# Kernel optimization log

Hardware: AMD Instinct MI355X
Metric: run time of the kernel (lower is better)

The kernel has to match this reference:

```python
import jax, jax.numpy as jnp
import numpy as np

N = 50000      # nodes
E = 800000     # edges
DIN = 128
DH = 128
DE = 128
DOUT = 2
EPS = 1e-5     # GraphNorm eps


def _xavier(key, fan_in, fan_out):
    lim = float(np.sqrt(6.0 / (fan_in + fan_out)))
    return jax.random.uniform(key, (fan_in, fan_out), jnp.float32, -lim, lim)


def setup_inputs() -> dict:
    key = jax.random.key(0)
    ks = jax.random.split(key, 8)
    x = jax.random.normal(ks[0], (N, DIN), jnp.float32)
    edge_index = jax.random.randint(ks[1], (2, E), 0, N, dtype=jnp.int32)
    W1 = _xavier(ks[2], DIN, DH); b1 = jnp.zeros((DH,), jnp.float32)
    W2 = _xavier(ks[3], DH, DH);  b2 = jnp.zeros((DH,), jnp.float32)
    W3 = _xavier(ks[4], DH, DE);  b3 = jnp.zeros((DE,), jnp.float32)
    gn1_w = jnp.ones((DH,), jnp.float32); gn1_b = jnp.zeros((DH,), jnp.float32); gn1_a = jnp.ones((DH,), jnp.float32)
    gn2_w = jnp.ones((DH,), jnp.float32); gn2_b = jnp.zeros((DH,), jnp.float32); gn2_a = jnp.ones((DH,), jnp.float32)
    Wout = _xavier(ks[5], DE, DOUT); bout = jnp.zeros((DOUT,), jnp.float32)
    return {
        "x": x, "edge_index": edge_index,
        "W1": W1, "b1": b1, "W2": W2, "b2": b2, "W3": W3, "b3": b3,
        "gn1_w": gn1_w, "gn1_b": gn1_b, "gn1_a": gn1_a,
        "gn2_w": gn2_w, "gn2_b": gn2_b, "gn2_a": gn2_a,
        "Wout": Wout, "bout": bout,
    }


def gcn_conv(x, src, dst, W, b):
    # PyG GCNConv: add self-loops, symmetric normalization, linear, scatter-add at dst.
    n = x.shape[0]
    h = x @ W                                   # [N, C]
    loop = jnp.arange(n, dtype=src.dtype)
    s = jnp.concatenate([src, loop])            # [E+N]
    d = jnp.concatenate([dst, loop])
    deg = jnp.zeros((n,), h.dtype).at[d].add(1.0)
    dinv = jnp.where(deg > 0, jax.lax.rsqrt(deg), 0.0)
    norm = dinv[s] * dinv[d]                    # [E+N]
    out = jnp.zeros_like(h).at[d].add(h[s] * norm[:, None])
    return out + b


def graph_norm(h, w, b, alpha):
    # Single-graph GraphNorm: shift by alpha*mean, normalize by variance of shifted values.
    mean = h.mean(axis=0)
    c = h - alpha * mean
    var = (c * c).mean(axis=0)
    return c * jax.lax.rsqrt(var + EPS) * w + b


def reference(x, edge_index, W1, b1, W2, b2, W3, b3,
              gn1_w, gn1_b, gn1_a, gn2_w, gn2_b, gn2_a, Wout, bout):
    src, dst = edge_index[0], edge_index[1]
    h = gcn_conv(x, src, dst, W1, b1)
    h = jax.nn.relu(graph_norm(h, gn1_w, gn1_b, gn1_a))   # dropout identity (eval)
    h = gcn_conv(h, src, dst, W2, b2)
    h = jax.nn.relu(graph_norm(h, gn2_w, gn2_b, gn2_a))
    h = gcn_conv(h, src, dst, W3, b3)
    return h @ Wout + bout
```

## Files before the change

kernel.cpp:

```cpp
#include <hip/hip_runtime.h>

#define GN_EPS 1e-5f


typedef __attribute__((ext_vector_type(8))) short short8;
typedef __attribute__((ext_vector_type(4))) float f32x4;

__device__ __forceinline__ unsigned short f2bf(float f) {
    unsigned u = __float_as_uint(f);
    u += 0x7fffu + ((u >> 16) & 1u);
    return (unsigned short)(u >> 16);
}
__device__ __forceinline__ float bflo(unsigned u) { return __uint_as_float(u << 16); }
__device__ __forceinline__ float bfhi(unsigned u) { return __uint_as_float(u & 0xffff0000u); }

__global__ void k_degi(const int* __restrict__ dst, int* __restrict__ degi,
                       unsigned short* __restrict__ slot, int e) {
    int i = blockIdx.x * blockDim.x + threadIdx.x;
    if (i < e) slot[i] = (unsigned short)atomicAdd(&degi[dst[i]], 1);
}

#define SCAN_CHUNK 4096
__global__ __launch_bounds__(256) void k_blocksum(const int* __restrict__ degi,
                                                  int* __restrict__ partial, int n) {
    int base = blockIdx.x * SCAN_CHUNK + threadIdx.x * 16;
    int s = 0;
    #pragma unroll
    for (int q = 0; q < 16; ++q) {
        int i = base + q;
        if (i < n) s += (degi[i] + 15) & ~15;
    }
    #pragma unroll
    for (int off = 32; off; off >>= 1) s += __shfl_down(s, off);
    __shared__ int ws[4];
    if ((threadIdx.x & 63) == 0) ws[threadIdx.x >> 6] = s;
    __syncthreads();
    if (threadIdx.x == 0) partial[blockIdx.x] = ws[0] + ws[1] + ws[2] + ws[3];
}

__global__ __launch_bounds__(256) void k_scanfinal(const int* __restrict__ degi,
                                                   const int* __restrict__ partial,
                                                   int* __restrict__ rowptr,
                                                   float* __restrict__ dinv, int n, int nb) {
    int blockbase = 0;
    for (int i = 0; i < (int)blockIdx.x; ++i) blockbase += partial[i];

    int base = blockIdx.x * SCAN_CHUNK + threadIdx.x * 16;
    int v[16], pv[16];
    int s = 0;
    #pragma unroll
    for (int q = 0; q < 16; ++q) {
        int i = base + q;
        v[q] = (i < n) ? degi[i] : 0;
        pv[q] = (v[q] + 15) & ~15;
        s += pv[q];
    }
    const int lane = threadIdx.x & 63;
    const int wid = threadIdx.x >> 6;
    int x = s;
    #pragma unroll
    for (int off = 1; off < 64; off <<= 1) {
        int t = __shfl_up(x, off);
        if (lane >= off) x += t;
    }
    __shared__ int ws[4];
    if (lane == 63) ws[wid] = x;
    __syncthreads();
    int waveoff = 0;
    if (wid > 0) waveoff += ws[0];
    if (wid > 1) waveoff += ws[1];
    if (wid > 2) waveoff += ws[2];
    int excl = x - s + waveoff + blockbase;
    #pragma unroll
    for (int q = 0; q < 16; ++q) {
        int i = base + q;
        if (i < n) {
            rowptr[i] = excl;
            dinv[i] = rsqrtf((float)(v[q] + 1));
        }
        excl += pv[q];
    }
    if ((int)blockIdx.x == nb - 1 && threadIdx.x == 255) {
        rowptr[n] = excl;
    }
}

__global__ void k_fill(const int* __restrict__ src, const int* __restrict__ dst,
                       const unsigned short* __restrict__ slot, const int* __restrict__ rowptr,
                       const float* __restrict__ dinv,
                       unsigned* __restrict__ csr_ew, int e) {
    int i = blockIdx.x * blockDim.x + threadIdx.x;
    if (i < e) {
        int s = src[i], d = dst[i];
        float w = dinv[s] * dinv[d];
        csr_ew[rowptr[d] + (int)slot[i]] = ((unsigned)s << 16) | (unsigned)f2bf(w);
    }
}

__global__ __launch_bounds__(256) void k_prep(const float* __restrict__ W1,
                                              const float* __restrict__ W2,
                                              const float* __restrict__ W3,
                                              const float* __restrict__ Wo,
                                              const float* __restrict__ b3,
                                              const float* __restrict__ bo,
                                              unsigned short* __restrict__ Wt,
                                              float* __restrict__ M,
                                              float* __restrict__ mb) {
    __shared__ unsigned short sT[128 * 130];
    if (blockIdx.x < 2) {
        const float* W = blockIdx.x == 0 ? W1 : W2;
        unsigned short* o = Wt + blockIdx.x * 16384;
        const float4* W4 = (const float4*)W;
        for (int idx = threadIdx.x; idx < 128 * 32; idx += 256) {
            int k = idx >> 5, c4 = idx & 31;
            float4 v = W4[k * 32 + c4];
            sT[(c4 * 4 + 0) * 130 + k] = f2bf(v.x);
            sT[(c4 * 4 + 1) * 130 + k] = f2bf(v.y);
            sT[(c4 * 4 + 2) * 130 + k] = f2bf(v.z);
            sT[(c4 * 4 + 3) * 130 + k] = f2bf(v.w);
        }
        __syncthreads();
        for (int idx = threadIdx.x; idx < 128 * 128; idx += 256) {
            int c = idx >> 7, k = idx & 127;
            o[idx] = sT[c * 130 + k];
        }
    } else {
        int k = threadIdx.x;
        if (k < 128) {
            float m0 = 0.f, m1 = 0.f;
            for (int c = 0; c < 128; ++c) {
                float w = W3[k * 128 + c];
                m0 += w * Wo[c * 2];
                m1 += w * Wo[c * 2 + 1];
            }
            M[k * 2] = m0;
            M[k * 2 + 1] = m1;
            if (k < 2) {
                float s = 0.f;
                for (int c = 0; c < 128; ++c) s += b3[c] * Wo[c * 2 + k];
                mb[k] = s + bo[k];
            }
        }
    }
}

#define LDK 136
__global__ __launch_bounds__(256) void k_gemm_f32(const float* __restrict__ X,
                                                  const unsigned short* __restrict__ Wt,
                                                  unsigned short* __restrict__ Y,
                                                  int nrows) {
    __shared__ __align__(16) unsigned short sX[64 * LDK];
    __shared__ __align__(16) unsigned short sB[128 * LDK];
    const int t = threadIdx.x;
    const int row0 = blockIdx.x * 64;

    for (int idx = t; idx < 128 * 16; idx += 256) {
        int c = idx >> 4, ch = idx & 15;
        uint4 v = ((const uint4*)(Wt + c * 128))[ch];
        *(uint4*)(&sB[c * LDK + ch * 8]) = v;
    }
    for (int idx = t; idx < 64 * 32; idx += 256) {
        int r = idx >> 5, c4 = idx & 31;
        int grow = row0 + r;
        float4 v = make_float4(0.f, 0.f, 0.f, 0.f);
        if (grow < nrows) v = ((const float4*)(X + (size_t)grow * 128))[c4];
        ushort4 o;
        o.x = f2bf(v.x); o.y = f2bf(v.y); o.z = f2bf(v.z); o.w = f2bf(v.w);
        *(ushort4*)(&sX[r * LDK + c4 * 4]) = o;
    }
    __syncthreads();

    const int w = t >> 6;
    const int lane = t & 63;
    const int m = lane & 15;
    const int quad = lane >> 4;

    f32x4 acc[8] = {};
    #pragma unroll
    for (int ks = 0; ks < 4; ++ks) {
        int ko = ks * 32 + quad * 8;
        short8 a = *(const short8*)(&sX[(w * 16 + m) * LDK + ko]);
        #pragma unroll
        for (int ct = 0; ct < 8; ++ct) {
            short8 b = *(const short8*)(&sB[(ct * 16 + m) * LDK + ko]);
            acc[ct] = __builtin_amdgcn_mfma_f32_16x16x32_bf16(a, b, acc[ct], 0, 0, 0);
        }
    }
    #pragma unroll
    for (int r = 0; r < 4; ++r) {
        int grow = row0 + w * 16 + quad * 4 + r;
        if (grow >= nrows) continue;
        unsigned short* yr = Y + (size_t)grow * 128 + m;
        #pragma unroll
        for (int ct = 0; ct < 8; ++ct) yr[ct * 16] = f2bf(acc[ct][r]);
    }
}

__global__ __launch_bounds__(256) void k_gemm_bf(const unsigned short* __restrict__ Xb,
                                                 const unsigned short* __restrict__ Wt,
                                                 unsigned short* __restrict__ Y,
                                                 const float* __restrict__ cs,
                                                 const float* __restrict__ cb,
                                                 int nrows) {
    __shared__ __align__(16) unsigned short sX[64 * LDK];
    __shared__ __align__(16) unsigned short sB[128 * LDK];
    const int t = threadIdx.x;
    const int row0 = blockIdx.x * 64;
// ... 26 lines not shown

    f32x4 acc[8] = {};
    #pragma unroll
    for (int ks = 0; ks < 4; ++ks) {
        int ko = ks * 32 + quad * 8;
        short8 a = *(const short8*)(&sX[(w * 16 + m) * LDK + ko]);
        #pragma unroll
        for (int ct = 0; ct < 8; ++ct) {
            short8 b = *(const short8*)(&sB[(ct * 16 + m) * LDK + ko]);
            acc[ct] = __builtin_amdgcn_mfma_f32_16x16x32_bf16(a, b, acc[ct], 0, 0, 0);
        }
    }
    #pragma unroll
    for (int r = 0; r < 4; ++r) {
        int grow = row0 + w * 16 + quad * 4 + r;
        if (grow >= nrows) continue;
        unsigned short* yr = Y + (size_t)grow * 128 + m;
        #pragma unroll
        for (int ct = 0; ct < 8; ++ct) yr[ct * 16] = f2bf(acc[ct][r]);
    }
}

__global__ __launch_bounds__(256) void k_gather(const unsigned short* __restrict__ H,
                                                unsigned short* __restrict__ O,
                                                const int* __restrict__ rowptr,
                                                const unsigned* __restrict__ csr_ew,
                                                const float* __restrict__ dinv,
                                                const float* __restrict__ bias,
                                                float* __restrict__ pS,
                                                float* __restrict__ pQ, int n) {
    __shared__ float sS[4][128];
    __shared__ float sQ[4][128];
    const int wid = threadIdx.x >> 6;
    const int node = blockIdx.x * 4 + wid;
    const int lane = threadIdx.x & 63;
    const int qw = lane >> 4;
    const int ql = lane & 15;
    const uint4* Hx = (const uint4*)H;
    float acc[8] = {};
    if (node < n) {
        float di = dinv[node];
        if (qw == 0) {
            uint4 u = Hx[(size_t)node * 16 + ql];
            float dd = di * di;
            float4 ba = ((const float4*)bias)[ql * 2];
            float4 bb = ((const float4*)bias)[ql * 2 + 1];
            acc[0] = bflo(u.x) * dd + ba.x; acc[1] = bfhi(u.x) * dd + ba.y;
            acc[2] = bflo(u.y) * dd + ba.z; acc[3] = bfhi(u.y) * dd + ba.w;
            acc[4] = bflo(u.z) * dd + bb.x; acc[5] = bfhi(u.z) * dd + bb.y;
            acc[6] = bflo(u.w) * dd + bb.z; acc[7] = bfhi(u.w) * dd + bb.w;
        }
        int j = rowptr[node];
        const int end = rowptr[node + 1];
        for (; j < end; j += 16) {
            unsigned ew[4];
            #pragma unroll
            for (int q = 0; q < 4; ++q) ew[q] = csr_ew[j + 4 * q + qw];
            uint4 u[4];
            #pragma unroll
            for (int q = 0; q < 4; ++q) {
                unsigned idx = ((ew[q] >> 12) & 0xFFFF0u) + (unsigned)ql;
                u[q] = Hx[idx];
            }
            #pragma unroll
            for (int q = 0; q < 4; ++q) {
                float nr = __uint_as_float(ew[q] << 16);
                acc[0] += bflo(u[q].x) * nr; acc[1] += bfhi(u[q].x) * nr;
                acc[2] += bflo(u[q].y) * nr; acc[3] += bfhi(u[q].y) * nr;
                acc[4] += bflo(u[q].z) * nr; acc[5] += bfhi(u[q].z) * nr;
                acc[6] += bflo(u[q].w) * nr; acc[7] += bfhi(u[q].w) * nr;
            }
        }
        #pragma unroll
        for (int i = 0; i < 8; ++i) {
            acc[i] += __shfl_down(acc[i], 32);
            acc[i] += __shfl_down(acc[i], 16);
        }
    }
    if (qw == 0) {
        if (node < n) {
            unsigned short h[8];
            float v[8];
            #pragma unroll
            for (int i = 0; i < 8; ++i) {
                h[i] = f2bf(acc[i]);
                v[i] = __uint_as_float((unsigned)h[i] << 16);
                sS[wid][ql * 8 + i] = v[i];
                sQ[wid][ql * 8 + i] = v[i] * v[i];
            }
            uint4 o;
            o.x = (unsigned)h[0] | ((unsigned)h[1] << 16);
            o.y = (unsigned)h[2] | ((unsigned)h[3] << 16);
            o.z = (unsigned)h[4] | ((unsigned)h[5] << 16);
            o.w = (unsigned)h[6] | ((unsigned)h[7] << 16);
            *(uint4*)(O + (size_t)node * 128 + ql * 8) = o;
        } else {
            #pragma unroll
            for (int i = 0; i < 8; ++i) {
                sS[wid][ql * 8 + i] = 0.f;
                sQ[wid][ql * 8 + i] = 0.f;
            }
        }
    }
    __syncthreads();
    const int t = threadIdx.x;
    if (t < 128) {
        float s = sS[0][t] + sS[1][t] + sS[2][t] + sS[3][t];
        float q = sQ[0][t] + sQ[1][t] + sQ[2][t] + sQ[3][t];
        const int slotb = (blockIdx.x & 63) << 7;
        atomicAdd(&pS[slotb + t], s);
        atomicAdd(&pQ[slotb + t], q);
    }
}

__global__ __launch_bounds__(256) void k_zproj(const unsigned short* __restrict__ Xb,
                                               const float* __restrict__ M,
                                               const float* __restrict__ cs,
                                               const float* __restrict__ cb,
                                               float2* __restrict__ Z, int n) {
    int node = blockIdx.x * 4 + (threadIdx.x >> 6);
    if (node >= n) return;
    int lane = threadIdx.x & 63;
    unsigned u = ((const unsigned*)Xb)[(size_t)node * 64 + lane];
// ... 48 lines not shown
        out[(size_t)node * 2 + 1] = acc.y;
    }
}

__global__ void k_finstats(const float* __restrict__ pS, const float* __restrict__ pQ,
                           const float* __restrict__ w, const float* __restrict__ b,
                           const float* __restrict__ alpha,
                           float* __restrict__ colscale, float* __restrict__ colshift,
                           int n) {
    int c = threadIdx.x;
    if (c >= 128) return;
    float s = 0.f, q = 0.f;
    #pragma unroll 8
    for (int blk = 0; blk < 64; ++blk) {
        s += pS[blk * 128 + c];
        q += pQ[blk * 128 + c];
    }
    float inv_n = 1.0f / (float)n;
    float m = s * inv_n;
    float eh2 = q * inv_n;
    float a = alpha[c];
    float var = eh2 - (2.0f * a - a * a) * m * m;
    float scale = rsqrtf(var + GN_EPS) * w[c];
    colscale[c] = scale;
    colshift[c] = b[c] - a * m * scale;
}

extern "C" void kernel_launch(void* const* d_in, const int* in_sizes, int n_in,
                              void* d_out, int out_size, void* d_ws, size_t ws_size,
                              hipStream_t stream) {
    const float* x    = (const float*)d_in[0];
    const int*   ei   = (const int*)  d_in[1];
    const float* W1   = (const float*)d_in[2];
    const float* b1   = (const float*)d_in[3];
    const float* W2   = (const float*)d_in[4];
    const float* b2   = (const float*)d_in[5];
    const float* W3   = (const float*)d_in[6];
    const float* b3   = (const float*)d_in[7];
    const float* gn1w = (const float*)d_in[8];
    const float* gn1b = (const float*)d_in[9];
    const float* gn1a = (const float*)d_in[10];
    const float* gn2w = (const float*)d_in[11];
    const float* gn2b = (const float*)d_in[12];
    const float* gn2a = (const float*)d_in[13];
    const float* Wout = (const float*)d_in[14];
    const float* bout = (const float*)d_in[15];
    float* out = (float*)d_out;

    const int n = in_sizes[0] / 128;
    const int e = in_sizes[1] / 2;
    const int* srcI = ei;
    const int* dstI = ei + e;

    char* base = (char*)d_ws;
    size_t off = 0;
    auto take = [&](size_t bytes) -> void* {
        void* r = base + off;
        off += (bytes + 15) & ~(size_t)15;
        return r;
    };
    unsigned short* bufH = (unsigned short*)take((size_t)n * 256);
    unsigned short* bufG = (unsigned short*)take((size_t)n * 256);
    float* dinv     = (float*)take((size_t)n * 4);
    float* colscale = (float*)take(128 * 4);
    float* colshift = (float*)take(128 * 4);
    int*   rowptr   = (int*)take(((size_t)n + 1) * 4);
    int*   partial  = (int*)take(64 * 4);
    unsigned short* Wt = (unsigned short*)take(2 * 16384 * 2);
    float* M        = (float*)take(256 * 4);
    float* mb       = (float*)take(2 * 4);
    float2* Z       = (float2*)take((size_t)n * 8);
    int*   degi     = (int*)take((size_t)n * 4);
    float* pS       = (float*)take(2 * 64 * 128 * 4);
    float* pQ       = (float*)take(2 * 64 * 128 * 4);
    size_t csr_cap  = (size_t)e + 16 * (size_t)n;
    unsigned* csr_ew = (unsigned*)take(csr_cap * 4);
    size_t zbytes   = (size_t)((base + off) - (char*)degi);

    unsigned short* slot = bufH;

    const int nb = (n + SCAN_CHUNK - 1) / SCAN_CHUNK;

    hipMemsetAsync(degi, 0, zbytes, stream);
    k_degi<<<(e + 255) / 256, 256, 0, stream>>>(dstI, degi, slot, e);
    k_blocksum<<<nb, 256, 0, stream>>>(degi, partial, n);
    k_scanfinal<<<nb, 256, 0, stream>>>(degi, partial, rowptr, dinv, n, nb);
    k_fill<<<(e + 255) / 256, 256, 0, stream>>>(srcI, dstI, slot, rowptr, dinv, csr_ew, e);
    k_prep<<<3, 256, 0, stream>>>(W1, W2, W3, Wout, b3, bout, Wt, M, mb);

    const int gemmGrid = (n + 63) / 64;
    const int gathGrid = (n + 3) / 4;

    k_gemm_f32<<<gemmGrid, 256, 0, stream>>>(x, Wt, bufH, n);
    k_gather<<<gathGrid, 256, 0, stream>>>(bufH, bufG, rowptr, csr_ew, dinv, b1, pS, pQ, n);
    k_finstats<<<1, 128, 0, stream>>>(pS, pQ, gn1w, gn1b, gn1a, colscale, colshift, n);

    k_gemm_bf<<<gemmGrid, 256, 0, stream>>>(bufG, Wt + 16384, bufH, colscale, colshift, n);
    k_gather<<<gathGrid, 256, 0, stream>>>(bufH, bufG, rowptr, csr_ew, dinv, b2,
                                           pS + 8192, pQ + 8192, n);
    k_finstats<<<1, 128, 0, stream>>>(pS + 8192, pQ + 8192, gn2w, gn2b, gn2a,
                                      colscale, colshift, n);

    k_zproj<<<gathGrid, 256, 0, stream>>>(bufG, M, colscale, colshift, Z, n);
    k_gatherZ<<<(n + 15) / 16, 256, 0, stream>>>(Z, rowptr, csr_ew, dinv, mb, out, n);
}
```

Measured before the change: 289.8 us.

## Fuse degree count into prep and CSR fill into first GEMM launch

Merges the weight-prep kernel with the degree-counting atomics, and runs the CSR fill and the first feature GEMM as interleaved block roles of a single launch. The fill now takes slot positions from a per-row atomic cursor instead of a precomputed slot array, and each thread handles four edges with vectorized index loads. This cuts kernel launches and lets the atomic-bound fill overlap the compute-bound GEMM. In exchange, edge order within each CSR row becomes nondeterministic, adds a rowcur buffer, and puts atomics back on the fill path.

New measurement: 301.9 us. +4.2%, slower.

```diff
diff --git a/kernel.cpp b/kernel.cpp
--- a/kernel.cpp
+++ b/kernel.cpp
@@ -14,98 +14,17 @@
 __device__ __forceinline__ float bflo(unsigned u) { return __uint_as_float(u << 16); }
 __device__ __forceinline__ float bfhi(unsigned u) { return __uint_as_float(u & 0xffff0000u); }
 
-__global__ void k_degi(const int* __restrict__ dst, int* __restrict__ degi,
-                       unsigned short* __restrict__ slot, int e) {
-    int i = blockIdx.x * blockDim.x + threadIdx.x;
-    if (i < e) slot[i] = (unsigned short)atomicAdd(&degi[dst[i]], 1);
-}
-
-#define SCAN_CHUNK 4096
-__global__ __launch_bounds__(256) void k_blocksum(const int* __restrict__ degi,
-                                                  int* __restrict__ partial, int n) {
-    int base = blockIdx.x * SCAN_CHUNK + threadIdx.x * 16;
-    int s = 0;
-    #pragma unroll
-    for (int q = 0; q < 16; ++q) {
-        int i = base + q;
-        if (i < n) s += (degi[i] + 15) & ~15;
-    }
-    #pragma unroll
-    for (int off = 32; off; off >>= 1) s += __shfl_down(s, off);
-    __shared__ int ws[4];
-    if ((threadIdx.x & 63) == 0) ws[threadIdx.x >> 6] = s;
-    __syncthreads();
-    if (threadIdx.x == 0) partial[blockIdx.x] = ws[0] + ws[1] + ws[2] + ws[3];
-}
-
-__global__ __launch_bounds__(256) void k_scanfinal(const int* __restrict__ degi,
-                                                   const int* __restrict__ partial,
-                                                   int* __restrict__ rowptr,
-                                                   float* __restrict__ dinv, int n, int nb) {
-    int blockbase = 0;
-    for (int i = 0; i < (int)blockIdx.x; ++i) blockbase += partial[i];
-
-    int base = blockIdx.x * SCAN_CHUNK + threadIdx.x * 16;
-    int v[16], pv[16];
-    int s = 0;
-    #pragma unroll
-    for (int q = 0; q < 16; ++q) {
-        int i = base + q;
-        v[q] = (i < n) ? degi[i] : 0;
-        pv[q] = (v[q] + 15) & ~15;
-        s += pv[q];
-    }
-    const int lane = threadIdx.x & 63;
-    const int wid = threadIdx.x >> 6;
-    int x = s;
-    #pragma unroll
-    for (int off = 1; off < 64; off <<= 1) {
-        int t = __shfl_up(x, off);
-        if (lane >= off) x += t;
-    }
-    __shared__ int ws[4];
-    if (lane == 63) ws[wid] = x;
-    __syncthreads();
-    int waveoff = 0;
-    if (wid > 0) waveoff += ws[0];
-    if (wid > 1) waveoff += ws[1];
-    if (wid > 2) waveoff += ws[2];
-    int excl = x - s + waveoff + blockbase;
-    #pragma unroll
-    for (int q = 0; q < 16; ++q) {
-        int i = base + q;
-        if (i < n) {
-            rowptr[i] = excl;
-            dinv[i] = rsqrtf((float)(v[q] + 1));
-        }
-        excl += pv[q];
-    }
-    if ((int)blockIdx.x == nb - 1 && threadIdx.x == 255) {
-        rowptr[n] = excl;
-    }
-}
-
-__global__ void k_fill(const int* __restrict__ src, const int* __restrict__ dst,
-                       const unsigned short* __restrict__ slot, const int* __restrict__ rowptr,
-                       const float* __restrict__ dinv,
-                       unsigned* __restrict__ csr_ew, int e) {
-    int i = blockIdx.x * blockDim.x + threadIdx.x;
-    if (i < e) {
-        int s = src[i], d = dst[i];
-        float w = dinv[s] * dinv[d];
-        csr_ew[rowptr[d] + (int)slot[i]] = ((unsigned)s << 16) | (unsigned)f2bf(w);
-    }
-}
-
-__global__ __launch_bounds__(256) void k_prep(const float* __restrict__ W1,
-                                              const float* __restrict__ W2,
-                                              const float* __restrict__ W3,
-                                              const float* __restrict__ Wo,
-                                              const float* __restrict__ b3,
-                                              const float* __restrict__ bo,
-                                              unsigned short* __restrict__ Wt,
-                                              float* __restrict__ M,
-                                              float* __restrict__ mb) {
+__global__ __launch_bounds__(256) void k_prep_count(const float* __restrict__ W1,
+                                                    const float* __restrict__ W2,
+                                                    const float* __restrict__ W3,
+                                                    const float* __restrict__ Wo,
+                                                    const float* __restrict__ b3,
+                                                    const float* __restrict__ bo,
+                                                    unsigned short* __restrict__ Wt,
+                                                    float* __restrict__ M,
+                                                    float* __restrict__ mb,
+                                                    const int* __restrict__ dst,
+                                                    int* __restrict__ degi, int e) {
     __shared__ unsigned short sT[128 * 130];
     if (blockIdx.x < 2) {
         const float* W = blockIdx.x == 0 ? W1 : W2;
@@ -124,7 +43,7 @@
             int c = idx >> 7, k = idx & 127;
             o[idx] = sT[c * 130 + k];
         }
-    } else {
+    } else if (blockIdx.x == 2) {
         int k = threadIdx.x;
         if (k < 128) {
             float m0 = 0.f, m1 = 0.f;
@@ -141,18 +60,147 @@
                 mb[k] = s + bo[k];
             }
         }
+    } else {
+        int base = ((int)(blockIdx.x - 3) * 256 + (int)threadIdx.x) * 4;
+        if (base + 3 < e && (((size_t)dst & 15) == 0)) {
+            int4 d = *(const int4*)(dst + base);
+            atomicAdd(&degi[d.x], 1);
+            atomicAdd(&degi[d.y], 1);
+            atomicAdd(&degi[d.z], 1);
+            atomicAdd(&degi[d.w], 1);
+        } else {
+            for (int i = base; i < e && i < base + 4; ++i) atomicAdd(&degi[dst[i]], 1);
+        }
+    }
+}
+
+#define SCAN_CHUNK 4096
+__global__ __launch_bounds__(256) void k_blocksum(const int* __restrict__ degi,
+                                                  int* __restrict__ partial, int n) {
+    int base = blockIdx.x * SCAN_CHUNK + threadIdx.x * 16;
+    int s = 0;
+    #pragma unroll
+    for (int q = 0; q < 16; ++q) {
+        int i = base + q;
+        if (i < n) s += (degi[i] + 15) & ~15;
+    }
+    #pragma unroll
+    for (int off = 32; off; off >>= 1) s += __shfl_down(s, off);
+    __shared__ int ws[4];
+    if ((threadIdx.x & 63) == 0) ws[threadIdx.x >> 6] = s;
+    __syncthreads();
+    if (threadIdx.x == 0) partial[blockIdx.x] = ws[0] + ws[1] + ws[2] + ws[3];
+}
+
+__global__ __launch_bounds__(256) void k_scanfinal(const int* __restrict__ degi,
+                                                   const int* __restrict__ partial,
+                                                   int* __restrict__ rowptr,
+                                                   int* __restrict__ rowcur,
+                                                   float* __restrict__ dinv, int n, int nb) {
+    int blockbase = 0;
+    for (int i = 0; i < (int)blockIdx.x; ++i) blockbase += partial[i];
+
+    int base = blockIdx.x * SCAN_CHUNK + threadIdx.x * 16;
+    int v[16], pv[16];
+    int s = 0;
+    #pragma unroll
+    for (int q = 0; q < 16; ++q) {
+        int i = base + q;
+        v[q] = (i < n) ? degi[i] : 0;
+        pv[q] = (v[q] + 15) & ~15;
+        s += pv[q];
+    }
+    const int lane = threadIdx.x & 63;
+    const int wid = threadIdx.x >> 6;
+    int x = s;
+    #pragma unroll
+    for (int off = 1; off < 64; off <<= 1) {
+        int t = __shfl_up(x, off);
+        if (lane >= off) x += t;
+    }
+    __shared__ int ws[4];
+    if (lane == 63) ws[wid] = x;
+    __syncthreads();
+    int waveoff = 0;
+    if (wid > 0) waveoff += ws[0];
+    if (wid > 1) waveoff += ws[1];
+    if (wid > 2) waveoff += ws[2];
+    int excl = x - s + waveoff + blockbase;
+    #pragma unroll
+    for (int q = 0; q < 16; ++q) {
+        int i = base + q;
+        if (i < n) {
+            rowptr[i] = excl;
+            rowcur[i] = excl;
+            dinv[i] = rsqrtf((float)(v[q] + 1));
+        }
+        excl += pv[q];
+    }
+    if ((int)blockIdx.x == nb - 1 && threadIdx.x == 255) {
+        rowptr[n] = excl;
     }
 }
 
 #define LDK 136
-__global__ __launch_bounds__(256) void k_gemm_f32(const float* __restrict__ X,
-                                                  const unsigned short* __restrict__ Wt,
-                                                  unsigned short* __restrict__ Y,
-                                                  int nrows) {
+
+__device__ __forceinline__ void fill_one(int s, int d,
+                                         int* __restrict__ rowcur,
+                                         const float* __restrict__ dinv,
+                                         unsigned* __restrict__ csr_ew) {
+    float w = dinv[s] * dinv[d];
+    int pos = atomicAdd(&rowcur[d], 1);
+    csr_ew[pos] = ((unsigned)s << 16) | (unsigned)f2bf(w);
+}
+
+__global__ __launch_bounds__(256) void k_fill_gemm(const float* __restrict__ X,
+                                                   const unsigned short* __restrict__ Wt,
+                                                   unsigned short* __restrict__ Y,
+                                                   const int* __restrict__ src,
+                                                   const int* __restrict__ dst,
+                                                   int* __restrict__ rowcur,
+                                                   const float* __restrict__ dinv,
+                                                   unsigned* __restrict__ csr_ew,
+                                                   int nrows, int e,
+                                                   int ngemm, int nfill) {
     __shared__ __align__(16) unsigned short sX[64 * LDK];
     __shared__ __align__(16) unsigned short sB[128 * LDK];
+
+    int mn2 = (ngemm < nfill ? ngemm : nfill) * 2;
+    bool isg;
+    int bid;
+    if ((int)blockIdx.x < mn2) {
+        isg = (blockIdx.x & 1) == 0;
+        bid = blockIdx.x >> 1;
+    } else {
+        int r = (int)blockIdx.x - mn2;
+        isg = ngemm > nfill;
+        bid = (mn2 >> 1) + r;
+    }
+
+    if (!isg) {
+        int base = (bid * 256 + (int)threadIdx.x) * 4;
+        if (base + 3 < e && (((size_t)src & 15) == 0) && (((size_t)dst & 15) == 0)) {
+            int4 s4 = *(const int4*)(src + base);
+            int4 d4 = *(const int4*)(dst + base);
+            float as0 = dinv[s4.x], as1 = dinv[s4.y], as2 = dinv[s4.z], as3 = dinv[s4.w];
+            float ad0 = dinv[d4.x], ad1 = dinv[d4.y], ad2 = dinv[d4.z], ad3 = dinv[d4.w];
+            int p0 = atomicAdd(&rowcur[d4.x], 1);
+            int p1 = atomicAdd(&rowcur[d4.y], 1);
+            int p2 = atomicAdd(&rowcur[d4.z], 1);
+            int p3 = atomicAdd(&rowcur[d4.w], 1);
+            csr_ew[p0] = ((unsigned)s4.x << 16) | (unsigned)f2bf(as0 * ad0);
+            csr_ew[p1] = ((unsigned)s4.y << 16) | (unsigned)f2bf(as1 * ad1);
+            csr_ew[p2] = ((unsigned)s4.z << 16) | (unsigned)f2bf(as2 * ad2);
+            csr_ew[p3] = ((unsigned)s4.w << 16) | (unsigned)f2bf(as3 * ad3);
+        } else {
+            for (int i = base; i < e && i < base + 4; ++i)
+                fill_one(src[i], dst[i], rowcur, dinv, csr_ew);
+        }
+        return;
+    }
+
     const int t = threadIdx.x;
-    const int row0 = blockIdx.x * 64;
+    const int row0 = bid * 64;
 
     for (int idx = t; idx < 128 * 16; idx += 256) {
         int c = idx >> 4, ch = idx & 15;
@@ -469,6 +517,7 @@
     float* colscale = (float*)take(128 * 4);
     float* colshift = (float*)take(128 * 4);
     int*   rowptr   = (int*)take(((size_t)n + 1) * 4);
+    int*   rowcur   = (int*)take((size_t)n * 4);
     int*   partial  = (int*)take(64 * 4);
     unsigned short* Wt = (unsigned short*)take(2 * 16384 * 2);
     float* M        = (float*)take(256 * 4);
@@ -481,21 +530,21 @@
     unsigned* csr_ew = (unsigned*)take(csr_cap * 4);
     size_t zbytes   = (size_t)((base + off) - (char*)degi);
 
-    unsigned short* slot = bufH;
-
     const int nb = (n + SCAN_CHUNK - 1) / SCAN_CHUNK;
+    const int countGrid = (e + 1023) / 1024;
+    const int gemmGrid = (n + 63) / 64;
+    const int fillGrid = (e + 1023) / 1024;
+    const int gathGrid = (n + 3) / 4;
 
     hipMemsetAsync(degi, 0, zbytes, stream);
-    k_degi<<<(e + 255) / 256, 256, 0, stream>>>(dstI, degi, slot, e);
+    k_prep_count<<<3 + countGrid, 256, 0, stream>>>(W1, W2, W3, Wout, b3, bout,
+                                                    Wt, M, mb, dstI, degi, e);
     k_blocksum<<<nb, 256, 0, stream>>>(degi, partial, n);
-    k_scanfinal<<<nb, 256, 0, stream>>>(degi, partial, rowptr, dinv, n, nb);
-    k_fill<<<(e + 255) / 256, 256, 0, stream>>>(srcI, dstI, slot, rowptr, dinv, csr_ew, e);
-    k_prep<<<3, 256, 0, stream>>>(W1, W2, W3, Wout, b3, bout, Wt, M, mb);
-
-    const int gemmGrid = (n + 63) / 64;
-    const int gathGrid = (n + 3) / 4;
-
-    k_gemm_f32<<<gemmGrid, 256, 0, stream>>>(x, Wt, bufH, n);
+    k_scanfinal<<<nb, 256, 0, stream>>>(degi, partial, rowptr, rowcur, dinv, n, nb);
+
+    k_fill_gemm<<<gemmGrid + fillGrid, 256, 0, stream>>>(x, Wt, bufH, srcI, dstI,
+                                                         rowcur, dinv, csr_ew,
+                                                         n, e, gemmGrid, fillGrid);
     k_gather<<<gathGrid, 256, 0, stream>>>(bufH, bufG, rowptr, csr_ew, dinv, b1, pS, pQ, n);
     k_finstats<<<1, 128, 0, stream>>>(pS, pQ, gn1w, gn1b, gn1a, colscale, colshift, n);
 
```

## Fuse weight prep with degree counting, vectorize CSR fill, prefetch edges in gather

Applied to the files above, without the earlier changes.

Merges the weight-transpose/projection prep kernel and the degree-counting atomic kernel into one launch, with each counting thread handling four edges through a vectorized dst load. The CSR fill kernel likewise processes four edges per thread using int4 loads. The gather loop is software-pipelined so the next batch of packed edge words loads while the current feature rows are accumulated. This is meant to cut launch overhead and hide edge-load latency in the gather, at the cost of fewer threads in the atomic and fill phases and more registers in the gather.

New measurement: 289.6 us. Within noise of the previous version (-0.1%).

```diff
diff --git a/kernel.cpp b/kernel.cpp
--- a/kernel.cpp
+++ b/kernel.cpp
@@ -14,98 +14,19 @@
 __device__ __forceinline__ float bflo(unsigned u) { return __uint_as_float(u << 16); }
 __device__ __forceinline__ float bfhi(unsigned u) { return __uint_as_float(u & 0xffff0000u); }
 
-__global__ void k_degi(const int* __restrict__ dst, int* __restrict__ degi,
-                       unsigned short* __restrict__ slot, int e) {
-    int i = blockIdx.x * blockDim.x + threadIdx.x;
-    if (i < e) slot[i] = (unsigned short)atomicAdd(&degi[dst[i]], 1);
-}
-
-#define SCAN_CHUNK 4096
-__global__ __launch_bounds__(256) void k_blocksum(const int* __restrict__ degi,
-                                                  int* __restrict__ partial, int n) {
-    int base = blockIdx.x * SCAN_CHUNK + threadIdx.x * 16;
-    int s = 0;
-    #pragma unroll
-    for (int q = 0; q < 16; ++q) {
-        int i = base + q;
-        if (i < n) s += (degi[i] + 15) & ~15;
-    }
-    #pragma unroll
-    for (int off = 32; off; off >>= 1) s += __shfl_down(s, off);
-    __shared__ int ws[4];
-    if ((threadIdx.x & 63) == 0) ws[threadIdx.x >> 6] = s;
-    __syncthreads();
-    if (threadIdx.x == 0) partial[blockIdx.x] = ws[0] + ws[1] + ws[2] + ws[3];
-}
-
-__global__ __launch_bounds__(256) void k_scanfinal(const int* __restrict__ degi,
-                                                   const int* __restrict__ partial,
-                                                   int* __restrict__ rowptr,
-                                                   float* __restrict__ dinv, int n, int nb) {
-    int blockbase = 0;
-    for (int i = 0; i < (int)blockIdx.x; ++i) blockbase += partial[i];
-
-    int base = blockIdx.x * SCAN_CHUNK + threadIdx.x * 16;
-    int v[16], pv[16];
-    int s = 0;
-    #pragma unroll
-    for (int q = 0; q < 16; ++q) {
-        int i = base + q;
-        v[q] = (i < n) ? degi[i] : 0;
-        pv[q] = (v[q] + 15) & ~15;
-        s += pv[q];
-    }
-    const int lane = threadIdx.x & 63;
-    const int wid = threadIdx.x >> 6;
-    int x = s;
-    #pragma unroll
-    for (int off = 1; off < 64; off <<= 1) {
-        int t = __shfl_up(x, off);
-        if (lane >= off) x += t;
-    }
-    __shared__ int ws[4];
-    if (lane == 63) ws[wid] = x;
-    __syncthreads();
-    int waveoff = 0;
-    if (wid > 0) waveoff += ws[0];
-    if (wid > 1) waveoff += ws[1];
-    if (wid > 2) waveoff += ws[2];
-    int excl = x - s + waveoff + blockbase;
-    #pragma unroll
-    for (int q = 0; q < 16; ++q) {
-        int i = base + q;
-        if (i < n) {
-            rowptr[i] = excl;
-            dinv[i] = rsqrtf((float)(v[q] + 1));
-        }
-        excl += pv[q];
-    }
-    if ((int)blockIdx.x == nb - 1 && threadIdx.x == 255) {
-        rowptr[n] = excl;
-    }
-}
-
-__global__ void k_fill(const int* __restrict__ src, const int* __restrict__ dst,
-                       const unsigned short* __restrict__ slot, const int* __restrict__ rowptr,
-                       const float* __restrict__ dinv,
-                       unsigned* __restrict__ csr_ew, int e) {
-    int i = blockIdx.x * blockDim.x + threadIdx.x;
-    if (i < e) {
-        int s = src[i], d = dst[i];
-        float w = dinv[s] * dinv[d];
-        csr_ew[rowptr[d] + (int)slot[i]] = ((unsigned)s << 16) | (unsigned)f2bf(w);
-    }
-}
-
-__global__ __launch_bounds__(256) void k_prep(const float* __restrict__ W1,
-                                              const float* __restrict__ W2,
-                                              const float* __restrict__ W3,
-                                              const float* __restrict__ Wo,
-                                              const float* __restrict__ b3,
-                                              const float* __restrict__ bo,
-                                              unsigned short* __restrict__ Wt,
-                                              float* __restrict__ M,
-                                              float* __restrict__ mb) {
+__global__ __launch_bounds__(256) void k_prep_degi(const float* __restrict__ W1,
+                                                   const float* __restrict__ W2,
+                                                   const float* __restrict__ W3,
+                                                   const float* __restrict__ Wo,
+                                                   const float* __restrict__ b3,
+                                                   const float* __restrict__ bo,
+                                                   unsigned short* __restrict__ Wt,
+                                                   float* __restrict__ M,
+                                                   float* __restrict__ mb,
+                                                   const int* __restrict__ dst,
+                                                   int* __restrict__ degi,
+                                                   unsigned short* __restrict__ slot,
+                                                   int e) {
     __shared__ unsigned short sT[128 * 130];
     if (blockIdx.x < 2) {
         const float* W = blockIdx.x == 0 ? W1 : W2;
@@ -124,7 +45,7 @@
             int c = idx >> 7, k = idx & 127;
             o[idx] = sT[c * 130 + k];
         }
-    } else {
+    } else if (blockIdx.x == 2) {
         int k = threadIdx.x;
         if (k < 128) {
             float m0 = 0.f, m1 = 0.f;
@@ -140,6 +61,112 @@
                 for (int c = 0; c < 128; ++c) s += b3[c] * Wo[c * 2 + k];
                 mb[k] = s + bo[k];
             }
+        }
+    } else {
+        int base = ((int)(blockIdx.x - 3) * 256 + (int)threadIdx.x) * 4;
+        if (base + 3 < e && (((size_t)dst & 15) == 0)) {
+            int4 d = *(const int4*)(dst + base);
+            int s0 = atomicAdd(&degi[d.x], 1);
+            int s1 = atomicAdd(&degi[d.y], 1);
+            int s2 = atomicAdd(&degi[d.z], 1);
+            int s3 = atomicAdd(&degi[d.w], 1);
+            ushort4 sl;
+            sl.x = (unsigned short)s0; sl.y = (unsigned short)s1;
+            sl.z = (unsigned short)s2; sl.w = (unsigned short)s3;
+            *(ushort4*)(slot + base) = sl;
+        } else {
+            for (int i = base; i < e && i < base + 4; ++i)
+                slot[i] = (unsigned short)atomicAdd(&degi[dst[i]], 1);
+        }
+    }
+}
+
+#define SCAN_CHUNK 4096
+__global__ __launch_bounds__(256) void k_blocksum(const int* __restrict__ degi,
+                                                  int* __restrict__ partial, int n) {
+    int base = blockIdx.x * SCAN_CHUNK + threadIdx.x * 16;
+    int s = 0;
+    #pragma unroll
+    for (int q = 0; q < 16; ++q) {
+        int i = base + q;
+        if (i < n) s += (degi[i] + 15) & ~15;
+    }
+    #pragma unroll
+    for (int off = 32; off; off >>= 1) s += __shfl_down(s, off);
+    __shared__ int ws[4];
+    if ((threadIdx.x & 63) == 0) ws[threadIdx.x >> 6] = s;
+    __syncthreads();
+    if (threadIdx.x == 0) partial[blockIdx.x] = ws[0] + ws[1] + ws[2] + ws[3];
+}
+
+__global__ __launch_bounds__(256) void k_scanfinal(const int* __restrict__ degi,
+                                                   const int* __restrict__ partial,
+                                                   int* __restrict__ rowptr,
+                                                   float* __restrict__ dinv, int n, int nb) {
+    int blockbase = 0;
+    for (int i = 0; i < (int)blockIdx.x; ++i) blockbase += partial[i];
+
+    int base = blockIdx.x * SCAN_CHUNK + threadIdx.x * 16;
+    int v[16], pv[16];
+    int s = 0;
+    #pragma unroll
+    for (int q = 0; q < 16; ++q) {
+        int i = base + q;
+        v[q] = (i < n) ? degi[i] : 0;
+        pv[q] = (v[q] + 15) & ~15;
+        s += pv[q];
+    }
+    const int lane = threadIdx.x & 63;
+    const int wid = threadIdx.x >> 6;
+    int x = s;
+    #pragma unroll
+    for (int off = 1; off < 64; off <<= 1) {
+        int t = __shfl_up(x, off);
+        if (lane >= off) x += t;
+    }
+    __shared__ int ws[4];
+    if (lane == 63) ws[wid] = x;
+    __syncthreads();
+    int waveoff = 0;
+    if (wid > 0) waveoff += ws[0];
+    if (wid > 1) waveoff += ws[1];
+    if (wid > 2) waveoff += ws[2];
+    int excl = x - s + waveoff + blockbase;
+    #pragma unroll
+    for (int q = 0; q < 16; ++q) {
+        int i = base + q;
+        if (i < n) {
+            rowptr[i] = excl;
+            dinv[i] = rsqrtf((float)(v[q] + 1));
+        }
+        excl += pv[q];
+    }
+    if ((int)blockIdx.x == nb - 1 && threadIdx.x == 255) {
+        rowptr[n] = excl;
+    }
+}
+
+__global__ void k_fill(const int* __restrict__ src, const int* __restrict__ dst,
+                       const unsigned short* __restrict__ slot, const int* __restrict__ rowptr,
+                       const float* __restrict__ dinv,
+                       unsigned* __restrict__ csr_ew, int e) {
+    int base = (blockIdx.x * blockDim.x + threadIdx.x) * 4;
+    if (base + 3 < e && (((size_t)src & 15) == 0) && (((size_t)dst & 15) == 0)) {
+        int4 s4 = *(const int4*)(src + base);
+        int4 d4 = *(const int4*)(dst + base);
+        ushort4 sl = *(const ushort4*)(slot + base);
+        float as0 = dinv[s4.x], as1 = dinv[s4.y], as2 = dinv[s4.z], as3 = dinv[s4.w];
+        float ad0 = dinv[d4.x], ad1 = dinv[d4.y], ad2 = dinv[d4.z], ad3 = dinv[d4.w];
+        int r0 = rowptr[d4.x], r1 = rowptr[d4.y], r2 = rowptr[d4.z], r3 = rowptr[d4.w];
+        csr_ew[r0 + sl.x] = ((unsigned)s4.x << 16) | (unsigned)f2bf(as0 * ad0);
+        csr_ew[r1 + sl.y] = ((unsigned)s4.y << 16) | (unsigned)f2bf(as1 * ad1);
+        csr_ew[r2 + sl.z] = ((unsigned)s4.z << 16) | (unsigned)f2bf(as2 * ad2);
+        csr_ew[r3 + sl.w] = ((unsigned)s4.w << 16) | (unsigned)f2bf(as3 * ad3);
+    } else {
+        for (int i = base; i < e && i < base + 4; ++i) {
+            int s = src[i], d = dst[i];
+            float w = dinv[s] * dinv[d];
+            csr_ew[rowptr[d] + (int)slot[i]] = ((unsigned)s << 16) | (unsigned)f2bf(w);
         }
     }
 }
@@ -285,23 +312,42 @@
         }
         int j = rowptr[node];
         const int end = rowptr[node + 1];
-        for (; j < end; j += 16) {
-            unsigned ew[4];
+        if (j < end) {
+            unsigned ewc[4];
             #pragma unroll
-            for (int q = 0; q < 4; ++q) ew[q] = csr_ew[j + 4 * q + qw];
-            uint4 u[4];
-            #pragma unroll
-            for (int q = 0; q < 4; ++q) {
-                unsigned idx = ((ew[q] >> 12) & 0xFFFF0u) + (unsigned)ql;
-                u[q] = Hx[idx];
+            for (int q = 0; q < 4; ++q) ewc[q] = csr_ew[j + 4 * q + qw];
+            for (j += 16; j < end; j += 16) {
+                uint4 u[4];
+                #pragma unroll
+                for (int q = 0; q < 4; ++q)
+                    u[q] = Hx[((ewc[q] >> 12) & 0xFFFF0u) + (unsigned)ql];
+                unsigned ewn[4];
+                #pragma unroll
+                for (int q = 0; q < 4; ++q) ewn[q] = csr_ew[j + 4 * q + qw];
+                #pragma unroll
+                for (int q = 0; q < 4; ++q) {
+                    float nr = __uint_as_float(ewc[q] << 16);
+                    acc[0] += bflo(u[q].x) * nr; acc[1] += bfhi(u[q].x) * nr;
+                    acc[2] += bflo(u[q].y) * nr; acc[3] += bfhi(u[q].y) * nr;
+                    acc[4] += bflo(u[q].z) * nr; acc[5] += bfhi(u[q].z) * nr;
+                    acc[6] += bflo(u[q].w) * nr; acc[7] += bfhi(u[q].w) * nr;
+                }
+                #pragma unroll
+                for (int q = 0; q < 4; ++q) ewc[q] = ewn[q];
             }
-            #pragma unroll
-            for (int q = 0; q < 4; ++q) {
-                float nr = __uint_as_float(ew[q] << 16);
-                acc[0] += bflo(u[q].x) * nr; acc[1] += bfhi(u[q].x) * nr;
-                acc[2] += bflo(u[q].y) * nr; acc[3] += bfhi(u[q].y) * nr;
-                acc[4] += bflo(u[q].z) * nr; acc[5] += bfhi(u[q].z) * nr;
-                acc[6] += bflo(u[q].w) * nr; acc[7] += bfhi(u[q].w) * nr;
+            {
+                uint4 u[4];
+                #pragma unroll
+                for (int q = 0; q < 4; ++q)
+                    u[q] = Hx[((ewc[q] >> 12) & 0xFFFF0u) + (unsigned)ql];
+                #pragma unroll
+                for (int q = 0; q < 4; ++q) {
+                    float nr = __uint_as_float(ewc[q] << 16);
+                    acc[0] += bflo(u[q].x) * nr; acc[1] += bfhi(u[q].x) * nr;
+                    acc[2] += bflo(u[q].y) * nr; acc[3] += bfhi(u[q].y) * nr;
+                    acc[4] += bflo(u[q].z) * nr; acc[5] += bfhi(u[q].z) * nr;
+                    acc[6] += bflo(u[q].w) * nr; acc[7] += bfhi(u[q].w) * nr;
+                }
             }
         }
         #pragma unroll
@@ -484,16 +530,16 @@
     unsigned short* slot = bufH;
 
     const int nb = (n + SCAN_CHUNK - 1) / SCAN_CHUNK;
+    const int countGrid = (e + 1023) / 1024;
+    const int gemmGrid = (n + 63) / 64;
+    const int gathGrid = (n + 3) / 4;
 
     hipMemsetAsync(degi, 0, zbytes, stream);
-    k_degi<<<(e + 255) / 256, 256, 0, stream>>>(dstI, degi, slot, e);
+    k_prep_degi<<<3 + countGrid, 256, 0, stream>>>(W1, W2, W3, Wout, b3, bout,
+                                                   Wt, M, mb, dstI, degi, slot, e);
     k_blocksum<<<nb, 256, 0, stream>>>(degi, partial, n);
     k_scanfinal<<<nb, 256, 0, stream>>>(degi, partial, rowptr, dinv, n, nb);
-    k_fill<<<(e + 255) / 256, 256, 0, stream>>>(srcI, dstI, slot, rowptr, dinv, csr_ew, e);
-    k_prep<<<3, 256, 0, stream>>>(W1, W2, W3, Wout, b3, bout, Wt, M, mb);
-
-    const int gemmGrid = (n + 63) / 64;
-    const int gathGrid = (n + 3) / 4;
+    k_fill<<<(e + 1023) / 1024, 256, 0, stream>>>(srcI, dstI, slot, rowptr, dinv, csr_ew, e);
 
     k_gemm_f32<<<gemmGrid, 256, 0, stream>>>(x, Wt, bufH, n);
     k_gather<<<gathGrid, 256, 0, stream>>>(bufH, bufG, rowptr, csr_ew, dinv, b1, pS, pQ, n);
```

## Build CSR via per-chunk LDS histograms instead of global atomics

Applied to the files above, without the earlier changes.

Replaces the global-atomic degree count with 64 chunked shared-memory histograms using packed 16-bit counters. A reduce kernel then turns the per-chunk counts into prefix offsets, and the fill kernel combines rowptr, chunk prefix and local position. It also merges this into the weight-prep launch, cuts row padding from 16 to 8 with a half-sized tail in the gather loop, and vectorizes the fill. The cost is an extra count buffer of nchunks*n shorts plus a reduce pass. Rows may now contain up to 7 padding slots, so the zero padding in csr_ew must still be present.

After: 270.0 us. 6.8% less time.

```diff
diff --git a/kernel.cpp b/kernel.cpp
--- a/kernel.cpp
+++ b/kernel.cpp
@@ -2,6 +2,10 @@
 
 #define GN_EPS 1e-5f
 
+
+#define HIST_C 64
+#define SCAN_CHUNK 4096
+#define LDK 136
 
 typedef __attribute__((ext_vector_type(8))) short short8;
 typedef __attribute__((ext_vector_type(4))) float f32x4;
@@ -14,100 +18,22 @@
 __device__ __forceinline__ float bflo(unsigned u) { return __uint_as_float(u << 16); }
 __device__ __forceinline__ float bfhi(unsigned u) { return __uint_as_float(u & 0xffff0000u); }
 
-__global__ void k_degi(const int* __restrict__ dst, int* __restrict__ degi,
-                       unsigned short* __restrict__ slot, int e) {
-    int i = blockIdx.x * blockDim.x + threadIdx.x;
-    if (i < e) slot[i] = (unsigned short)atomicAdd(&degi[dst[i]], 1);
-}
-
-#define SCAN_CHUNK 4096
-__global__ __launch_bounds__(256) void k_blocksum(const int* __restrict__ degi,
-                                                  int* __restrict__ partial, int n) {
-    int base = blockIdx.x * SCAN_CHUNK + threadIdx.x * 16;
-    int s = 0;
-    #pragma unroll
-    for (int q = 0; q < 16; ++q) {
-        int i = base + q;
-        if (i < n) s += (degi[i] + 15) & ~15;
-    }
-    #pragma unroll
-    for (int off = 32; off; off >>= 1) s += __shfl_down(s, off);
-    __shared__ int ws[4];
-    if ((threadIdx.x & 63) == 0) ws[threadIdx.x >> 6] = s;
-    __syncthreads();
-    if (threadIdx.x == 0) partial[blockIdx.x] = ws[0] + ws[1] + ws[2] + ws[3];
-}
-
-__global__ __launch_bounds__(256) void k_scanfinal(const int* __restrict__ degi,
-                                                   const int* __restrict__ partial,
-                                                   int* __restrict__ rowptr,
-                                                   float* __restrict__ dinv, int n, int nb) {
-    int blockbase = 0;
-    for (int i = 0; i < (int)blockIdx.x; ++i) blockbase += partial[i];
-
-    int base = blockIdx.x * SCAN_CHUNK + threadIdx.x * 16;
-    int v[16], pv[16];
-    int s = 0;
-    #pragma unroll
-    for (int q = 0; q < 16; ++q) {
-        int i = base + q;
-        v[q] = (i < n) ? degi[i] : 0;
-        pv[q] = (v[q] + 15) & ~15;
-        s += pv[q];
-    }
-    const int lane = threadIdx.x & 63;
-    const int wid = threadIdx.x >> 6;
-    int x = s;
-    #pragma unroll
-    for (int off = 1; off < 64; off <<= 1) {
-        int t = __shfl_up(x, off);
-        if (lane >= off) x += t;
-    }
-    __shared__ int ws[4];
-    if (lane == 63) ws[wid] = x;
-    __syncthreads();
-    int waveoff = 0;
-    if (wid > 0) waveoff += ws[0];
-    if (wid > 1) waveoff += ws[1];
-    if (wid > 2) waveoff += ws[2];
-    int excl = x - s + waveoff + blockbase;
-    #pragma unroll
-    for (int q = 0; q < 16; ++q) {
-        int i = base + q;
-        if (i < n) {
-            rowptr[i] = excl;
-            dinv[i] = rsqrtf((float)(v[q] + 1));
-        }
-        excl += pv[q];
-    }
-    if ((int)blockIdx.x == nb - 1 && threadIdx.x == 255) {
-        rowptr[n] = excl;
-    }
-}
-
-__global__ void k_fill(const int* __restrict__ src, const int* __restrict__ dst,
-                       const unsigned short* __restrict__ slot, const int* __restrict__ rowptr,
-                       const float* __restrict__ dinv,
-                       unsigned* __restrict__ csr_ew, int e) {
-    int i = blockIdx.x * blockDim.x + threadIdx.x;
-    if (i < e) {
-        int s = src[i], d = dst[i];
-        float w = dinv[s] * dinv[d];
-        csr_ew[rowptr[d] + (int)slot[i]] = ((unsigned)s << 16) | (unsigned)f2bf(w);
-    }
-}
-
-__global__ __launch_bounds__(256) void k_prep(const float* __restrict__ W1,
-                                              const float* __restrict__ W2,
-                                              const float* __restrict__ W3,
-                                              const float* __restrict__ Wo,
-                                              const float* __restrict__ b3,
-                                              const float* __restrict__ bo,
-                                              unsigned short* __restrict__ Wt,
-                                              float* __restrict__ M,
-                                              float* __restrict__ mb) {
-    __shared__ unsigned short sT[128 * 130];
+__global__ __launch_bounds__(256) void k_prep_hist(const float* __restrict__ W1,
+                                                   const float* __restrict__ W2,
+                                                   const float* __restrict__ W3,
+                                                   const float* __restrict__ Wo,
+                                                   const float* __restrict__ b3,
+                                                   const float* __restrict__ bo,
+                                                   unsigned short* __restrict__ Wt,
+                                                   float* __restrict__ M,
+                                                   float* __restrict__ mb,
+                                                   const int* __restrict__ dst,
+                                                   unsigned short* __restrict__ cnt,
+                                                   unsigned short* __restrict__ pos,
+                                                   int e, int n, int chunk) {
+    __shared__ __align__(16) unsigned bins[32768];
     if (blockIdx.x < 2) {
+        unsigned short* sT = (unsigned short*)bins;
         const float* W = blockIdx.x == 0 ? W1 : W2;
         unsigned short* o = Wt + blockIdx.x * 16384;
         const float4* W4 = (const float4*)W;
@@ -124,7 +50,7 @@
             int c = idx >> 7, k = idx & 127;
             o[idx] = sT[c * 130 + k];
         }
-    } else {
+    } else if (blockIdx.x == 2) {
         int k = threadIdx.x;
         if (k < 128) {
             float m0 = 0.f, m1 = 0.f;
@@ -141,10 +67,175 @@
                 mb[k] = s + bo[k];
             }
         }
-    }
-}
-
-#define LDK 136
+    } else {
+        const int c = (int)blockIdx.x - 3;
+        const int c0 = c * chunk;
+        const int c1 = (c0 + chunk < e) ? c0 + chunk : e;
+        const int nw = (n + 1) >> 1;
+        for (int i = threadIdx.x; i < nw; i += 256) bins[i] = 0u;
+        __syncthreads();
+        const bool al = ((size_t)dst & 15) == 0;
+        for (int i = c0 + (int)threadIdx.x * 4; i < c1; i += 1024) {
+            if (al && i + 3 < c1) {
+                int4 d4 = *(const int4*)(dst + i);
+                unsigned o0 = atomicAdd(&bins[(unsigned)d4.x >> 1],
+                                        (d4.x & 1) ? 0x10000u : 1u);
+                unsigned o1 = atomicAdd(&bins[(unsigned)d4.y >> 1],
+                                        (d4.y & 1) ? 0x10000u : 1u);
+                unsigned o2 = atomicAdd(&bins[(unsigned)d4.z >> 1],
+                                        (d4.z & 1) ? 0x10000u : 1u);
+                unsigned o3 = atomicAdd(&bins[(unsigned)d4.w >> 1],
+                                        (d4.w & 1) ? 0x10000u : 1u);
+                ushort4 p;
+                p.x = (unsigned short)((o0 >> ((d4.x & 1) * 16)) & 0xffffu);
+                p.y = (unsigned short)((o1 >> ((d4.y & 1) * 16)) & 0xffffu);
+                p.z = (unsigned short)((o2 >> ((d4.z & 1) * 16)) & 0xffffu);
+                p.w = (unsigned short)((o3 >> ((d4.w & 1) * 16)) & 0xffffu);
+                *(ushort4*)(pos + i) = p;
+            } else {
+                for (int k = i; k < c1 && k < i + 4; ++k) {
+                    int d = dst[k];
+                    unsigned old = atomicAdd(&bins[(unsigned)d >> 1],
+                                             (d & 1) ? 0x10000u : 1u);
+                    pos[k] = (unsigned short)((old >> ((d & 1) * 16)) & 0xffffu);
+                }
+            }
+        }
+        __syncthreads();
+        unsigned short* cr = cnt + (size_t)c * n;
+        if ((n & 1) == 0) {
+            unsigned* cr32 = (unsigned*)cr;
+            for (int i = threadIdx.x; i < (n >> 1); i += 256) cr32[i] = bins[i];
+        } else {
+            for (int i = threadIdx.x; i < n; i += 256)
+                cr[i] = (unsigned short)((bins[i >> 1] >> ((i & 1) * 16)) & 0xffffu);
+        }
+    }
+}
+
+__global__ __launch_bounds__(256) void k_reduce(unsigned short* __restrict__ cnt,
+                                                int* __restrict__ degi,
+                                                int n, int nchunks) {
+    int node = blockIdx.x * 256 + threadIdx.x;
+    if (node >= n) return;
+    int s = 0;
+    int cb = 0;
+    for (; cb + 8 <= nchunks; cb += 8) {
+        int v[8];
+        #pragma unroll
+        for (int q = 0; q < 8; ++q) v[q] = cnt[(size_t)(cb + q) * n + node];
+        #pragma unroll
+        for (int q = 0; q < 8; ++q) {
+            cnt[(size_t)(cb + q) * n + node] = (unsigned short)s;
+            s += v[q];
+        }
+    }
+    for (; cb < nchunks; ++cb) {
+        size_t id = (size_t)cb * n + node;
+        int v = cnt[id];
+        cnt[id] = (unsigned short)s;
+        s += v;
+    }
+    degi[node] = s;
+}
+
+__global__ __launch_bounds__(256) void k_blocksum(const int* __restrict__ degi,
+                                                  int* __restrict__ partial, int n) {
+    int base = blockIdx.x * SCAN_CHUNK + threadIdx.x * 16;
+    int s = 0;
+    #pragma unroll
+    for (int q = 0; q < 16; ++q) {
+        int i = base + q;
+        if (i < n) s += (degi[i] + 7) & ~7;
+    }
+    #pragma unroll
+    for (int off = 32; off; off >>= 1) s += __shfl_down(s, off);
+    __shared__ int ws[4];
+    if ((threadIdx.x & 63) == 0) ws[threadIdx.x >> 6] = s;
+    __syncthreads();
+    if (threadIdx.x == 0) partial[blockIdx.x] = ws[0] + ws[1] + ws[2] + ws[3];
+}
+
+__global__ __launch_bounds__(256) void k_scanfinal(const int* __restrict__ degi,
+                                                   const int* __restrict__ partial,
+                                                   int* __restrict__ rowptr,
+                                                   float* __restrict__ dinv, int n, int nb) {
+    int blockbase = 0;
+    for (int i = 0; i < (int)blockIdx.x; ++i) blockbase += partial[i];
+
+    int base = blockIdx.x * SCAN_CHUNK + threadIdx.x * 16;
+    int v[16], pv[16];
+    int s = 0;
+    #pragma unroll
+    for (int q = 0; q < 16; ++q) {
+        int i = base + q;
+        v[q] = (i < n) ? degi[i] : 0;
+        pv[q] = (v[q] + 7) & ~7;
+        s += pv[q];
+    }
+    const int lane = threadIdx.x & 63;
+    const int wid = threadIdx.x >> 6;
+    int x = s;
+    #pragma unroll
+    for (int off = 1; off < 64; off <<= 1) {
+        int t = __shfl_up(x, off);
+        if (lane >= off) x += t;
+    }
+    __shared__ int ws[4];
+    if (lane == 63) ws[wid] = x;
+    __syncthreads();
+    int waveoff = 0;
+    if (wid > 0) waveoff += ws[0];
+    if (wid > 1) waveoff += ws[1];
+    if (wid > 2) waveoff += ws[2];
+    int excl = x - s + waveoff + blockbase;
+    #pragma unroll
+    for (int q = 0; q < 16; ++q) {
+        int i = base + q;
+        if (i < n) {
+            rowptr[i] = excl;
+            dinv[i] = rsqrtf((float)(v[q] + 1));
+        }
+        excl += pv[q];
+    }
+    if ((int)blockIdx.x == nb - 1 && threadIdx.x == 255) {
+        rowptr[n] = excl;
+    }
+}
+
+__global__ void k_fill(const int* __restrict__ src, const int* __restrict__ dst,
+                       const unsigned short* __restrict__ pos,
+                       const unsigned short* __restrict__ pref,
+                       const int* __restrict__ rowptr,
+                       const float* __restrict__ dinv,
+                       unsigned* __restrict__ csr_ew, int e, int n, int chunk) {
+    int base = (blockIdx.x * blockDim.x + threadIdx.x) * 4;
+    if (base >= e) return;
+    const unsigned short* pr = pref + (size_t)(base / chunk) * n;
+    if (base + 3 < e && (((size_t)src & 15) == 0) && (((size_t)dst & 15) == 0)) {
+        int4 s4 = *(const int4*)(src + base);
+        int4 d4 = *(const int4*)(dst + base);
+        ushort4 p4 = *(const ushort4*)(pos + base);
+        float as0 = dinv[s4.x], as1 = dinv[s4.y], as2 = dinv[s4.z], as3 = dinv[s4.w];
+        float ad0 = dinv[d4.x], ad1 = dinv[d4.y], ad2 = dinv[d4.z], ad3 = dinv[d4.w];
+        int b0 = rowptr[d4.x] + pr[d4.x] + p4.x;
+        int b1 = rowptr[d4.y] + pr[d4.y] + p4.y;
+        int b2 = rowptr[d4.z] + pr[d4.z] + p4.z;
+        int b3 = rowptr[d4.w] + pr[d4.w] + p4.w;
+        csr_ew[b0] = ((unsigned)s4.x << 16) | (unsigned)f2bf(as0 * ad0);
+        csr_ew[b1] = ((unsigned)s4.y << 16) | (unsigned)f2bf(as1 * ad1);
+        csr_ew[b2] = ((unsigned)s4.z << 16) | (unsigned)f2bf(as2 * ad2);
+        csr_ew[b3] = ((unsigned)s4.w << 16) | (unsigned)f2bf(as3 * ad3);
+    } else {
+        for (int i = base; i < e && i < base + 4; ++i) {
+            int s = src[i], d = dst[i];
+            float w = dinv[s] * dinv[d];
+            csr_ew[rowptr[d] + (int)pr[d] + (int)pos[i]] =
+                ((unsigned)s << 16) | (unsigned)f2bf(w);
+        }
+    }
+}
+
 __global__ __launch_bounds__(256) void k_gemm_f32(const float* __restrict__ X,
                                                   const unsigned short* __restrict__ Wt,
                                                   unsigned short* __restrict__ Y,
@@ -285,18 +376,33 @@
         }
         int j = rowptr[node];
         const int end = rowptr[node + 1];
-        for (; j < end; j += 16) {
+        for (; j + 16 <= end; j += 16) {
             unsigned ew[4];
             #pragma unroll
             for (int q = 0; q < 4; ++q) ew[q] = csr_ew[j + 4 * q + qw];
             uint4 u[4];
             #pragma unroll
+            for (int q = 0; q < 4; ++q)
+                u[q] = Hx[((ew[q] >> 12) & 0xFFFF0u) + (unsigned)ql];
+            #pragma unroll
             for (int q = 0; q < 4; ++q) {
-                unsigned idx = ((ew[q] >> 12) & 0xFFFF0u) + (unsigned)ql;
-                u[q] = Hx[idx];
+                float nr = __uint_as_float(ew[q] << 16);
+                acc[0] += bflo(u[q].x) * nr; acc[1] += bfhi(u[q].x) * nr;
+                acc[2] += bflo(u[q].y) * nr; acc[3] += bfhi(u[q].y) * nr;
+                acc[4] += bflo(u[q].z) * nr; acc[5] += bfhi(u[q].z) * nr;
+                acc[6] += bflo(u[q].w) * nr; acc[7] += bfhi(u[q].w) * nr;
             }
-            #pragma unroll
-            for (int q = 0; q < 4; ++q) {
+        }
+        if (j < end) {
+            unsigned ew[2];
+            #pragma unroll
+            for (int q = 0; q < 2; ++q) ew[q] = csr_ew[j + qw * 2 + q];
+            uint4 u[2];
+            #pragma unroll
+            for (int q = 0; q < 2; ++q)
+                u[q] = Hx[((ew[q] >> 12) & 0xFFFF0u) + (unsigned)ql];
+            #pragma unroll
+            for (int q = 0; q < 2; ++q) {
                 float nr = __uint_as_float(ew[q] << 16);
                 acc[0] += bflo(u[q].x) * nr; acc[1] += bfhi(u[q].x) * nr;
                 acc[2] += bflo(u[q].y) * nr; acc[3] += bfhi(u[q].y) * nr;
@@ -456,6 +562,9 @@
     const int* srcI = ei;
     const int* dstI = ei + e;
 
+    const int chunk = (((e + HIST_C - 1) / HIST_C) + 3) & ~3;
+    const int nchunks = (e + chunk - 1) / chunk;
+
     char* base = (char*)d_ws;
     size_t off = 0;
     auto take = [&](size_t bytes) -> void* {
@@ -475,25 +584,26 @@
     float* mb       = (float*)take(2 * 4);
     float2* Z       = (float2*)take((size_t)n * 8);
     int*   degi     = (int*)take((size_t)n * 4);
+    unsigned short* cnt = (unsigned short*)take((size_t)nchunks * n * 2);
+    unsigned short* pos = (unsigned short*)take((size_t)e * 2);
     float* pS       = (float*)take(2 * 64 * 128 * 4);
     float* pQ       = (float*)take(2 * 64 * 128 * 4);
-    size_t csr_cap  = (size_t)e + 16 * (size_t)n;
+    size_t csr_cap  = (size_t)e + 8 * (size_t)n;
     unsigned* csr_ew = (unsigned*)take(csr_cap * 4);
-    size_t zbytes   = (size_t)((base + off) - (char*)degi);
-
-    unsigned short* slot = bufH;
+    size_t zbytes   = (size_t)((base + off) - (char*)pS);
 
     const int nb = (n + SCAN_CHUNK - 1) / SCAN_CHUNK;
-
-    hipMemsetAsync(degi, 0, zbytes, stream);
-    k_degi<<<(e + 255) / 256, 256, 0, stream>>>(dstI, degi, slot, e);
+    const int gemmGrid = (n + 63) / 64;
+    const int gathGrid = (n + 3) / 4;
+
+    hipMemsetAsync(pS, 0, zbytes, stream);
+    k_prep_hist<<<3 + nchunks, 256, 0, stream>>>(W1, W2, W3, Wout, b3, bout,
+                                                 Wt, M, mb, dstI, cnt, pos, e, n, chunk);
+    k_reduce<<<(n + 255) / 256, 256, 0, stream>>>(cnt, degi, n, nchunks);
     k_blocksum<<<nb, 256, 0, stream>>>(degi, partial, n);
     k_scanfinal<<<nb, 256, 0, stream>>>(degi, partial, rowptr, dinv, n, nb);
-    k_fill<<<(e + 255) / 256, 256, 0, stream>>>(srcI, dstI, slot, rowptr, dinv, csr_ew, e);
-    k_prep<<<3, 256, 0, stream>>>(W1, W2, W3, Wout, b3, bout, Wt, M, mb);
-
-    const int gemmGrid = (n + 63) / 64;
-    const int gathGrid = (n + 3) / 4;
+    k_fill<<<(e + 1023) / 1024, 256, 0, stream>>>(srcI, dstI, pos, cnt, rowptr,
+                                                  dinv, csr_ew, e, n, chunk);
 
     k_gemm_f32<<<gemmGrid, 256, 0, stream>>>(x, Wt, bufH, n);
     k_gather<<<gathGrid, 256, 0, stream>>>(bufH, bufG, rowptr, csr_ew, dinv, b1, pS, pQ, n);
```
